# Optimization experiments

Measured on AMD Instinct MI355X. Metric: run time of the kernel, lower is better.

The kernel has to match this reference:

```python
import jax, jax.numpy as jnp
import numpy as np

NUM_NODES = 100000
E = 512    # embedding_size
U = 64     # embedding_u_size
T = 8      # edge_type_count
A = 32     # dim_a
B = 8192   # batch
NB = 10    # neighbors per type


def setup_inputs() -> dict:
    key = jax.random.key(0)
    ks = jax.random.split(key, 8)
    std = 1.0 / np.sqrt(E)
    return {
        "node_embeddings": jax.random.uniform(ks[0], (NUM_NODES, E), jnp.float32, -1.0, 1.0),
        "node_type_embeddings": jax.random.uniform(ks[1], (NUM_NODES, T, U), jnp.float32, -1.0, 1.0),
        "trans_weights": jax.random.normal(ks[2], (T, U, E), jnp.float32) * std,
        "trans_weights_s1": jax.random.normal(ks[3], (T, U, A), jnp.float32) * std,
        "trans_weights_s2": jax.random.normal(ks[4], (T, A, 1), jnp.float32) * std,
        "train_inputs": jax.random.randint(ks[5], (B,), 0, NUM_NODES, jnp.int32),
        "train_types": jax.random.randint(ks[6], (B,), 0, T, jnp.int32),
        "node_neigh": jax.random.randint(ks[7], (B, T, NB), 0, NUM_NODES, jnp.int32),
    }


def reference(node_embeddings, node_type_embeddings, trans_weights,
              trans_weights_s1, trans_weights_s2,
              train_inputs, train_types, node_neigh):
    # node_embed: [B, E]
    node_embed = node_embeddings[train_inputs]
    # Per-type neighbor gather. Original materializes [B,T,NB,T,U] then takes the
    # diagonal over the two type axes; we gather only the diagonal directly:
    # neigh_embed[b,t,n,:] = node_type_embeddings[node_neigh[b,t,n], t, :]
    type_idx = jnp.arange(T)[None, :, None]              # [1,T,1]
    neigh_embed = node_type_embeddings[node_neigh, type_idx]  # [B,T,NB,U]
    node_type_embed = neigh_embed.sum(axis=2)            # [B,T,U]

    # Per-sample gathered projection weights (MoE-style by edge type)
    w_s1 = trans_weights_s1[train_types]                 # [B,U,A]
    w_s2 = trans_weights_s2[train_types]                 # [B,A,1]
    w = trans_weights[train_types]                       # [B,U,E]

    # attention over edge types
    h = jnp.tanh(jnp.einsum('btu,bua->bta', node_type_embed, w_s1))  # [B,T,A]
    scores = jnp.einsum('bta,bao->bt', h, w_s2)          # [B,T] (squeeze of [B,T,1])
    attention = jax.nn.softmax(scores, axis=-1)          # [B,T]

    agg = jnp.einsum('bt,btu->bu', attention, node_type_embed)  # [B,U]
    node_embed = node_embed + jnp.einsum('bu,bue->be', agg, w)  # [B,E]

    # F.normalize(dim=1): divide by L2 norm clamped at 1e-12
    norm = jnp.maximum(jnp.linalg.norm(node_embed, axis=1, keepdims=True), 1e-12)
    return node_embed / norm
```

## Files before the change

kernel.cpp:

```cpp
#include <hip/hip_runtime.h>

#define E_DIM 512
#define U_DIM 64
#define T_DIM 8
#define A_DIM 32
#define NB    10
#define BATCH 8192

__launch_bounds__(256, 4)
__global__ void gatne_kernel(
    const float* __restrict__ node_embeddings,
    const float* __restrict__ node_type_embeddings,
    const float* __restrict__ trans_weights,
    const float* __restrict__ trans_weights_s1,
    const float* __restrict__ trans_weights_s2,
    const int*   __restrict__ train_inputs,
    const int*   __restrict__ train_types,
    const int*   __restrict__ node_neigh,
    float*       __restrict__ out)
{
    const int b   = blockIdx.x;
    const int tid = threadIdx.x;

    __shared__ int   s_neigh[T_DIM * NB];
    __shared__ float s_nte[T_DIM][U_DIM];
    __shared__ float s_w1[U_DIM * A_DIM];
    __shared__ float s_w2[A_DIM];
    __shared__ float s_att[T_DIM];
    __shared__ float s_agg[U_DIM];
    __shared__ float s_red[4];

    const int ni = train_inputs[b];
    const int ty = train_types[b];

    if (tid < T_DIM * NB) s_neigh[tid] = node_neigh[b * (T_DIM * NB) + tid];
    for (int i = tid; i < U_DIM * A_DIM; i += 256)
        s_w1[i] = trans_weights_s1[ty * (U_DIM * A_DIM) + i];
    if (tid < A_DIM) s_w2[tid] = trans_weights_s2[ty * A_DIM + tid];
    __syncthreads();

    {
        const int u = tid & 63;
        const int g = tid >> 6;
        #pragma unroll
        for (int k = 0; k < 2; ++k) {
            const int t = g + 4 * k;
            float acc = 0.f;
            #pragma unroll
            for (int n = 0; n < NB; ++n) {
                const int nb = s_neigh[t * NB + n];
                acc += node_type_embeddings[(size_t)nb * (T_DIM * U_DIM) + t * U_DIM + u];
            }
            s_nte[t][u] = acc;
        }
    }
    __syncthreads();

    {
        const int t = tid >> 5;
        const int a = tid & 31;
        float hsum = 0.f;
        #pragma unroll
        for (int u = 0; u < U_DIM; ++u)
            hsum += s_nte[t][u] * s_w1[u * A_DIM + a];
        float val = tanhf(hsum) * s_w2[a];
        #pragma unroll
        for (int off = 16; off > 0; off >>= 1)
            val += __shfl_down(val, off, 32);
        if (a == 0) s_att[t] = val;
    }
    __syncthreads();

    if (tid == 0) {
        float m = s_att[0];
        #pragma unroll
        for (int t = 1; t < T_DIM; ++t) m = fmaxf(m, s_att[t]);
        float e[T_DIM], sum = 0.f;
        #pragma unroll
        for (int t = 0; t < T_DIM; ++t) { e[t] = __expf(s_att[t] - m); sum += e[t]; }
        const float inv = 1.f / sum;
        #pragma unroll
        for (int t = 0; t < T_DIM; ++t) s_att[t] = e[t] * inv;
    }
    __syncthreads();

    if (tid < U_DIM) {
        float acc = 0.f;
        #pragma unroll
        for (int t = 0; t < T_DIM; ++t)
            acc += s_att[t] * s_nte[t][tid];
        s_agg[tid] = acc;
    }
    __syncthreads();

    const int e0 = tid * 2;
    const float2 ne = *(const float2*)(node_embeddings + (size_t)ni * E_DIM + e0);
    float v0 = ne.x, v1 = ne.y;
    const float* wbase = trans_weights + (size_t)ty * (U_DIM * E_DIM) + e0;
    #pragma unroll 8
    for (int u = 0; u < U_DIM; ++u) {
        const float a = s_agg[u];
        const float2 wv = *(const float2*)(wbase + (size_t)u * E_DIM);
        v0 = fmaf(a, wv.x, v0);
        v1 = fmaf(a, wv.y, v1);
    }

    float ss = v0 * v0 + v1 * v1;
    #pragma unroll
    for (int off = 32; off > 0; off >>= 1)
        ss += __shfl_down(ss, off, 64);
    if ((tid & 63) == 0) s_red[tid >> 6] = ss;
    __syncthreads();
    const float total = s_red[0] + s_red[1] + s_red[2] + s_red[3];
    const float inv = 1.f / fmaxf(sqrtf(total), 1e-12f);

    float2 o; o.x = v0 * inv; o.y = v1 * inv;
    *(float2*)(out + (size_t)b * E_DIM + e0) = o;
}

extern "C" void kernel_launch(void* const* d_in, const int* in_sizes, int n_in,
                              void* d_out, int out_size, void* d_ws, size_t ws_size,
                              hipStream_t stream) {
    const float* node_embeddings      = (const float*)d_in[0];
    const float* node_type_embeddings = (const float*)d_in[1];
    const float* trans_weights        = (const float*)d_in[2];
    const float* trans_weights_s1     = (const float*)d_in[3];
    const float* trans_weights_s2     = (const float*)d_in[4];
    const int*   train_inputs         = (const int*)d_in[5];
    const int*   train_types          = (const int*)d_in[6];
    const int*   node_neigh           = (const int*)d_in[7];
    float* out = (float*)d_out;

    gatne_kernel<<<BATCH, 256, 0, stream>>>(
        node_embeddings, node_type_embeddings, trans_weights,
        trans_weights_s1, trans_weights_s2,
        train_inputs, train_types, node_neigh, out);
}
```

Baseline: 414.3 us.

## Bucket samples by edge type and process one sample per wavefront

Adds a bucketing kernel that groups batch indices by edge type using ballot and atomics. The main kernel then launches blocks per type, loads that type's attention weights once (transposed and padded in shared memory) and loops persistently over samples, handling one sample per wavefront. Softmax and aggregation are computed in registers, and the agg vector is broadcast with readlane, which removes several block-wide barriers. The aim is to reuse per-type weights across samples and cut synchronisation, at the cost of an extra kernel launch, a memset, and only 8×128 blocks, which may leave the GPU underutilised or imbalanced across types.

```diff
diff --git a/kernel.cpp b/kernel.cpp
--- a/kernel.cpp
+++ b/kernel.cpp
@@ -6,116 +6,164 @@
 #define A_DIM 32
 #define NB    10
 #define BATCH 8192
+#define BKT_STRIDE 8192
 
-__launch_bounds__(256, 4)
-__global__ void gatne_kernel(
+
+__global__ __launch_bounds__(256) void bucket_kernel(
+    const int* __restrict__ types, int* __restrict__ cnt, int* __restrict__ bkt)
+{
+    const int i = blockIdx.x * 256 + threadIdx.x;
+    const int ty = types[i];
+    const unsigned long long below = (1ull << (threadIdx.x & 63)) - 1;
+    #pragma unroll
+    for (int t = 0; t < T_DIM; ++t) {
+        unsigned long long m = __ballot(ty == t);
+        if (ty == t) {
+            int lead = __ffsll(m) - 1;
+            int base = 0;
+            if ((threadIdx.x & 63) == lead)
+                base = atomicAdd(&cnt[t], (int)__popcll(m));
+            base = __shfl(base, lead, 64);
+            bkt[t * BKT_STRIDE + base + (int)__popcll(m & below)] = i;
+        }
+    }
+}
+
+static __device__ __forceinline__ float bcast_lane(float x, int l) {
+    return __int_as_float(__builtin_amdgcn_readlane(__float_as_int(x), l));
+}
+
+__global__ __launch_bounds__(256) void gatne_main(
     const float* __restrict__ node_embeddings,
     const float* __restrict__ node_type_embeddings,
     const float* __restrict__ trans_weights,
     const float* __restrict__ trans_weights_s1,
     const float* __restrict__ trans_weights_s2,
     const int*   __restrict__ train_inputs,
-    const int*   __restrict__ train_types,
+    const int*   __restrict__ counts,
+    const int*   __restrict__ bkt,
     const int*   __restrict__ node_neigh,
     float*       __restrict__ out)
 {
-    const int b   = blockIdx.x;
-    const int tid = threadIdx.x;
+    const int ty    = blockIdx.x;
+    const int count = counts[ty];
+    if ((int)(blockIdx.y * 4) >= count) return;
 
-    __shared__ int   s_neigh[T_DIM * NB];
-    __shared__ float s_nte[T_DIM][U_DIM];
-    __shared__ float s_w1[U_DIM * A_DIM];
-    __shared__ float s_w2[A_DIM];
-    __shared__ float s_att[T_DIM];
-    __shared__ float s_agg[U_DIM];
-    __shared__ float s_red[4];
+    const int tid  = threadIdx.x;
+    const int lane = tid & 63;
+    const int w    = tid >> 6;
 
-    const int ni = train_inputs[b];
-    const int ty = train_types[b];
+    __shared__ __align__(16) float sW1T[A_DIM * 68];
+    __shared__ __align__(16) float sNte[4][T_DIM * 68];
+    __shared__ __align__(16) float sSc[4][8];
+    __shared__ float sW2[A_DIM];
+    __shared__ int   sNei[4][80];
 
-    if (tid < T_DIM * NB) s_neigh[tid] = node_neigh[b * (T_DIM * NB) + tid];
-    for (int i = tid; i < U_DIM * A_DIM; i += 256)
-        s_w1[i] = trans_weights_s1[ty * (U_DIM * A_DIM) + i];
-    if (tid < A_DIM) s_w2[tid] = trans_weights_s2[ty * A_DIM + tid];
+    for (int k = tid; k < U_DIM * A_DIM; k += 256) {
+        const int u = k >> 5, a = k & 31;
+        sW1T[a * 68 + u] = trans_weights_s1[ty * (U_DIM * A_DIM) + k];
+    }
+    if (tid < A_DIM) sW2[tid] = trans_weights_s2[ty * A_DIM + tid];
     __syncthreads();
 
-    {
-        const int u = tid & 63;
-        const int g = tid >> 6;
-        #pragma unroll
-        for (int k = 0; k < 2; ++k) {
-            const int t = g + 4 * k;
-            float acc = 0.f;
+    const float* Wty = trans_weights + (size_t)ty * (U_DIM * E_DIM);
+    const int t8 = lane >> 3;
+    const int a0 = lane & 7;
+
+    for (int j = blockIdx.y; j * 4 < count; j += gridDim.y) {
+        const int  si    = j * 4 + w;
+        const bool valid = si < count;
+        float agg = 0.f;
+        int s = 0, ni = 0;
+
+        if (valid) {
+            s  = bkt[ty * BKT_STRIDE + si];
+            ni = train_inputs[s];
+            {
+                const int* np = node_neigh + (size_t)s * (T_DIM * NB);
+                sNei[w][lane] = np[lane];
+                if (lane < 16) sNei[w][64 + lane] = np[64 + lane];
+            }
+            float acc[T_DIM];
             #pragma unroll
-            for (int n = 0; n < NB; ++n) {
-                const int nb = s_neigh[t * NB + n];
-                acc += node_type_embeddings[(size_t)nb * (T_DIM * U_DIM) + t * U_DIM + u];
+            for (int t = 0; t < T_DIM; ++t) {
+                float a = 0.f;
+                #pragma unroll
+                for (int n = 0; n < NB; ++n) {
+                    const int nb = sNei[w][t * NB + n];
+                    a += node_type_embeddings[(size_t)nb * (T_DIM * U_DIM) + t * U_DIM + lane];
+                }
+                acc[t] = a;
+                sNte[w][t * 68 + lane] = a;
             }
-            s_nte[t][u] = acc;
+            float h0 = 0.f, h1 = 0.f, h2 = 0.f, h3 = 0.f;
+            #pragma unroll
+            for (int uq = 0; uq < 16; ++uq) {
+                const float4 nv  = *(const float4*)&sNte[w][t8 * 68 + uq * 4];
+                const float4 wa  = *(const float4*)&sW1T[(a0     ) * 68 + uq * 4];
+                const float4 wb  = *(const float4*)&sW1T[(a0 +  8) * 68 + uq * 4];
+                const float4 wc  = *(const float4*)&sW1T[(a0 + 16) * 68 + uq * 4];
+                const float4 wd  = *(const float4*)&sW1T[(a0 + 24) * 68 + uq * 4];
+                h0 = fmaf(nv.x, wa.x, h0); h0 = fmaf(nv.y, wa.y, h0);
+                h0 = fmaf(nv.z, wa.z, h0); h0 = fmaf(nv.w, wa.w, h0);
+                h1 = fmaf(nv.x, wb.x, h1); h1 = fmaf(nv.y, wb.y, h1);
+                h1 = fmaf(nv.z, wb.z, h1); h1 = fmaf(nv.w, wb.w, h1);
+                h2 = fmaf(nv.x, wc.x, h2); h2 = fmaf(nv.y, wc.y, h2);
+                h2 = fmaf(nv.z, wc.z, h2); h2 = fmaf(nv.w, wc.w, h2);
+                h3 = fmaf(nv.x, wd.x, h3); h3 = fmaf(nv.y, wd.y, h3);
+                h3 = fmaf(nv.z, wd.z, h3); h3 = fmaf(nv.w, wd.w, h3);
+            }
+            float r = tanhf(h0) * sW2[a0]      + tanhf(h1) * sW2[a0 + 8]
+                    + tanhf(h2) * sW2[a0 + 16] + tanhf(h3) * sW2[a0 + 24];
+            r += __shfl_xor(r, 1, 64);
+            r += __shfl_xor(r, 2, 64);
+            r += __shfl_xor(r, 4, 64);
+            if (a0 == 0) sSc[w][t8] = r;
+            const float4 sc0 = *(const float4*)&sSc[w][0];
+            const float4 sc1 = *(const float4*)&sSc[w][4];
+            float mx = fmaxf(fmaxf(fmaxf(sc0.x, sc0.y), fmaxf(sc0.z, sc0.w)),
+                             fmaxf(fmaxf(sc1.x, sc1.y), fmaxf(sc1.z, sc1.w)));
+            const float e0 = __expf(sc0.x - mx), e1 = __expf(sc0.y - mx);
+            const float e2 = __expf(sc0.z - mx), e3 = __expf(sc0.w - mx);
+            const float e4 = __expf(sc1.x - mx), e5 = __expf(sc1.y - mx);
+            const float e6 = __expf(sc1.z - mx), e7 = __expf(sc1.w - mx);
+            const float inv = 1.f / (e0 + e1 + e2 + e3 + e4 + e5 + e6 + e7);
+            agg = (e0 * acc[0] + e1 * acc[1] + e2 * acc[2] + e3 * acc[3]
+                 + e4 * acc[4] + e5 * acc[5] + e6 * acc[6] + e7 * acc[7]) * inv;
+        }
+
+        __syncthreads();
+
+        if (valid) {
+            float v[8];
+            const float4* nr = (const float4*)(node_embeddings + (size_t)ni * E_DIM + lane * 8);
+            const float4 nv0 = nr[0], nv1 = nr[1];
+            v[0] = nv0.x; v[1] = nv0.y; v[2] = nv0.z; v[3] = nv0.w;
+            v[4] = nv1.x; v[5] = nv1.y; v[6] = nv1.z; v[7] = nv1.w;
+            const float* Wp = Wty + lane * 8;
+            #pragma unroll 8
+            for (int u = 0; u < U_DIM; ++u) {
+                const float au = bcast_lane(agg, u);
+                const float4 w0 = *(const float4*)(Wp + (size_t)u * E_DIM);
+                const float4 w1 = *(const float4*)(Wp + (size_t)u * E_DIM + 4);
+                v[0] = fmaf(au, w0.x, v[0]); v[1] = fmaf(au, w0.y, v[1]);
+                v[2] = fmaf(au, w0.z, v[2]); v[3] = fmaf(au, w0.w, v[3]);
+                v[4] = fmaf(au, w1.x, v[4]); v[5] = fmaf(au, w1.y, v[5]);
+                v[6] = fmaf(au, w1.z, v[6]); v[7] = fmaf(au, w1.w, v[7]);
+            }
+            float ss = v[0]*v[0] + v[1]*v[1] + v[2]*v[2] + v[3]*v[3]
+                     + v[4]*v[4] + v[5]*v[5] + v[6]*v[6] + v[7]*v[7];
+            #pragma unroll
+            for (int off = 1; off < 64; off <<= 1)
+                ss += __shfl_xor(ss, off, 64);
+            const float invn = 1.f / fmaxf(sqrtf(ss), 1e-12f);
+            float4 o0, o1;
+            o0.x = v[0]*invn; o0.y = v[1]*invn; o0.z = v[2]*invn; o0.w = v[3]*invn;
+            o1.x = v[4]*invn; o1.y = v[5]*invn; o1.z = v[6]*invn; o1.w = v[7]*invn;
+            float4* op = (float4*)(out + (size_t)s * E_DIM + lane * 8);
+            op[0] = o0; op[1] = o1;
         }
     }
-    __syncthreads();
-
-    {
-        const int t = tid >> 5;
-        const int a = tid & 31;
-        float hsum = 0.f;
-        #pragma unroll
-        for (int u = 0; u < U_DIM; ++u)
-            hsum += s_nte[t][u] * s_w1[u * A_DIM + a];
-        float val = tanhf(hsum) * s_w2[a];
-        #pragma unroll
-        for (int off = 16; off > 0; off >>= 1)
-            val += __shfl_down(val, off, 32);
-        if (a == 0) s_att[t] = val;
-    }
-    __syncthreads();
-
-    if (tid == 0) {
-        float m = s_att[0];
-        #pragma unroll
-        for (int t = 1; t < T_DIM; ++t) m = fmaxf(m, s_att[t]);
-        float e[T_DIM], sum = 0.f;
-        #pragma unroll
-        for (int t = 0; t < T_DIM; ++t) { e[t] = __expf(s_att[t] - m); sum += e[t]; }
-        const float inv = 1.f / sum;
-        #pragma unroll
-        for (int t = 0; t < T_DIM; ++t) s_att[t] = e[t] * inv;
-    }
-    __syncthreads();
-
-    if (tid < U_DIM) {
-        float acc = 0.f;
-        #pragma unroll
-        for (int t = 0; t < T_DIM; ++t)
-            acc += s_att[t] * s_nte[t][tid];
-        s_agg[tid] = acc;
-    }
-    __syncthreads();
-
-    const int e0 = tid * 2;
-    const float2 ne = *(const float2*)(node_embeddings + (size_t)ni * E_DIM + e0);
-    float v0 = ne.x, v1 = ne.y;
-    const float* wbase = trans_weights + (size_t)ty * (U_DIM * E_DIM) + e0;
-    #pragma unroll 8
-    for (int u = 0; u < U_DIM; ++u) {
-        const float a = s_agg[u];
-        const float2 wv = *(const float2*)(wbase + (size_t)u * E_DIM);
-        v0 = fmaf(a, wv.x, v0);
-        v1 = fmaf(a, wv.y, v1);
-    }
-
-    float ss = v0 * v0 + v1 * v1;
-    #pragma unroll
-    for (int off = 32; off > 0; off >>= 1)
-        ss += __shfl_down(ss, off, 64);
-    if ((tid & 63) == 0) s_red[tid >> 6] = ss;
-    __syncthreads();
-    const float total = s_red[0] + s_red[1] + s_red[2] + s_red[3];
-    const float inv = 1.f / fmaxf(sqrtf(total), 1e-12f);
-
-    float2 o; o.x = v0 * inv; o.y = v1 * inv;
-    *(float2*)(out + (size_t)b * E_DIM + e0) = o;
 }
 
 extern "C" void kernel_launch(void* const* d_in, const int* in_sizes, int n_in,
@@ -131,8 +179,13 @@
     const int*   node_neigh           = (const int*)d_in[7];
     float* out = (float*)d_out;
 
-    gatne_kernel<<<BATCH, 256, 0, stream>>>(
+    int* cnt = (int*)d_ws;
+    int* bkt = (int*)((char*)d_ws + 256);
+
+    hipMemsetAsync(cnt, 0, 32, stream);
+    bucket_kernel<<<BATCH / 256, 256, 0, stream>>>(train_types, cnt, bkt);
+    gatne_main<<<dim3(T_DIM, 128), 256, 0, stream>>>(
         node_embeddings, node_type_embeddings, trans_weights,
         trans_weights_s1, trans_weights_s2,
-        train_inputs, train_types, node_neigh, out);
+        train_inputs, cnt, bkt, node_neigh, out);
 }
```

Measured after the change: 430.2 us. 1.04x slower.
